# Kernel optimization log

Measured on AMD Instinct MI355X. Metric: run time of the kernel, lower is better.

Reference implementation:

```python
import jax, jax.numpy as jnp
import numpy as np

N_GENE = 50000
N_PROT = 50000
E = 500000
D = 128          # embedding_dim
C = 32           # out_channels = embedding_dim // attn_heads
F_IN = 256       # in_channels per node type
NUM_MP = 3       # metapaths: [gene-gene, gene-protein, protein-protein]


def _glorot(key, shape):
    lim = float(np.sqrt(6.0 / (shape[0] + shape[1])))
    return jax.random.uniform(key, shape, minval=-lim, maxval=lim, dtype=jnp.float32)


def setup_inputs() -> dict:
    key = jax.random.key(0)
    ks = jax.random.split(key, 24)
    inp = {
        "x_gene": jax.random.normal(ks[0], (N_GENE, F_IN), dtype=jnp.float32),
        "x_protein": jax.random.normal(ks[1], (N_PROT, F_IN), dtype=jnp.float32),
        # node-type projections linear_l / linear_r
        "Wl_gene": _glorot(ks[2], (D, F_IN)), "bl_gene": jnp.zeros((D,), jnp.float32),
        "Wr_gene": _glorot(ks[3], (D, F_IN)), "br_gene": jnp.zeros((D,), jnp.float32),
        "Wl_prot": _glorot(ks[4], (D, F_IN)), "bl_prot": jnp.zeros((D,), jnp.float32),
        "Wr_prot": _glorot(ks[5], (D, F_IN)), "br_prot": jnp.zeros((D,), jnp.float32),
        # per-metapath attention params (stacked over 3 metapaths)
        "alW": jnp.stack([_glorot(ks[6 + i], (C, D)) for i in range(NUM_MP)]),
        "alb": jnp.zeros((NUM_MP, C), jnp.float32),
        "arW": jnp.stack([_glorot(ks[9 + i], (C, D)) for i in range(NUM_MP)]),
        "arb": jnp.zeros((NUM_MP, C), jnp.float32),
        "qw": jnp.stack([_glorot(ks[12 + i], (2 * C, 1)) for i in range(NUM_MP)]),
        "sharp": jnp.ones((NUM_MP,), jnp.float32),  # 'sharpening' alpha_activation
        # per-node-type relation-weighting conv (Linear(D, 1))
        "conv_gene_W": _glorot(ks[15], (1, D)), "conv_gene_b": jnp.zeros((1,), jnp.float32),
        "conv_prot_W": _glorot(ks[16], (1, D)), "conv_prot_b": jnp.zeros((1,), jnp.float32),
        # edge indices: row 0 = head node (aggregation target), row 1 = tail node
        "edge_gg": jax.random.randint(ks[17], (2, E), 0, N_GENE, dtype=jnp.int32),
        "edge_gp": jnp.stack([jax.random.randint(ks[18], (E,), 0, N_GENE, dtype=jnp.int32),
                               jax.random.randint(ks[19], (E,), 0, N_PROT, dtype=jnp.int32)]),
        "edge_pp": jax.random.randint(ks[20], (2, E), 0, N_PROT, dtype=jnp.int32),
    }
    return inp


def _segment_softmax(scores, seg, n):
    # numerically stable softmax over variable-size neighborhoods (grouped by seg)
    m = jax.ops.segment_max(scores, seg, num_segments=n)
    m = jnp.where(jnp.isfinite(m), m, 0.0)
    ex = jnp.exp(scores - m[seg])
    denom = jax.ops.segment_sum(ex, seg, num_segments=n)
    return ex / (denom[seg] + 1e-16)


def _metapath_agg(l_head, r_tail, alW, alb, arW, arb, qw, sharp, eidx, n_head):
    # alpha_l / alpha_r node-level projections [N, C]
    al = l_head @ alW.T + alb
    ar = r_tail @ arW.T + arb
    src, dst = eidx[0], eidx[1]           # head (aggregate-at), tail (message-from)
    a_i = al[src]                          # [E, C]
    a_j = ar[dst]                          # [E, C]
    # attn_q: Tanh then Linear(2C -> 1, no bias); 'sharpening' scales the logit
    e = (jnp.tanh(jnp.concatenate([a_i, a_j], axis=1)) @ qw)[:, 0] * sharp  # [E]
    alpha = _segment_softmax(e, src, n_head)
    # message x_j * alpha, scatter-add into head nodes (aggr='add')
    return jax.ops.segment_sum(r_tail[dst] * alpha[:, None], src, num_segments=n_head)


def _relation_combine(aggs, l_self, conv_W, conv_b):
    # stack relation embeddings + self embedding: [N, R, D]
    out = jnp.stack(aggs + [l_self], axis=1)
    beta = jax.nn.softmax(out @ conv_W.T + conv_b, axis=1)  # [N, R, 1]
    return jax.nn.relu(jnp.sum(out * beta, axis=1))          # [N, D]


def reference(x_gene, x_protein, Wl_gene, bl_gene, Wr_gene, br_gene,
              Wl_prot, bl_prot, Wr_prot, br_prot,
              alW, alb, arW, arb, qw, sharp,
              conv_gene_W, conv_gene_b, conv_prot_W, conv_prot_b,
              edge_gg, edge_gp, edge_pp):
    # first layer: l/r projections from raw features
    l_gene = x_gene @ Wl_gene.T + bl_gene
    r_gene = x_gene @ Wr_gene.T + br_gene
    l_prot = x_protein @ Wl_prot.T + bl_prot
    r_prot = x_protein @ Wr_prot.T + br_prot

    # metapath 0: gene <- gene ; metapath 1: gene <- protein ; metapath 2: protein <- protein
    agg_gg = _metapath_agg(l_gene, r_gene, alW[0], alb[0], arW[0], arb[0], qw[0], sharp[0], edge_gg, N_GENE)
    agg_gp = _metapath_agg(l_gene, r_prot, alW[1], alb[1], arW[1], arb[1], qw[1], sharp[1], edge_gp, N_GENE)
    agg_pp = _metapath_agg(l_prot, r_prot, alW[2], alb[2], arW[2], arb[2], qw[2], sharp[2], edge_pp, N_PROT)

    out_gene = _relation_combine([agg_gg, agg_gp], l_gene, conv_gene_W, conv_gene_b)
    out_prot = _relation_combine([agg_pp], l_prot, conv_prot_W, conv_prot_b)
    return (out_gene, out_prot)
```

## Files before the change

### kernel.cpp

```cpp
#include <hip/hip_runtime.h>
#include <hip/hip_bf16.h>


typedef __attribute__((ext_vector_type(8))) short short8;
typedef __attribute__((ext_vector_type(4))) float floatx4;

__device__ __forceinline__ void gload16(const void* g, void* l) {
  __builtin_amdgcn_global_load_lds(
      (const __attribute__((address_space(1))) void*)g,
      (__attribute__((address_space(3))) void*)l, 16, 0, 0);
}

__device__ __forceinline__ ushort f2b(float x) {
  __hip_bfloat16 h = __float2bfloat16(x);
  return *reinterpret_cast<ushort*>(&h);
}
__device__ __forceinline__ float b2f_lo(unsigned v) { return __uint_as_float(v << 16); }
__device__ __forceinline__ float b2f_hi(unsigned v) { return __uint_as_float(v & 0xffff0000u); }

struct CvtArgs {
  const float* src[8];
  ushort* dst[8];
  int valid[8];
  int total[8];
  int bstart[9];
};
__global__ __launch_bounds__(256) void cvt_multi(CvtArgs a) {
  int b = blockIdx.x;
  int e = 0;
#pragma unroll
  for (int j = 1; j < 8; ++j)
    if (b >= a.bstart[j]) e = j;
  int i = ((b - a.bstart[e]) * 256 + threadIdx.x) * 4;
  if (i >= a.total[e]) return;
  float4 v = make_float4(0.f, 0.f, 0.f, 0.f);
  if (i < a.valid[e]) v = *(const float4*)(a.src[e] + i);
  ushort4 o;
  o.x = f2b(v.x); o.y = f2b(v.y); o.z = f2b(v.z); o.w = f2b(v.w);
  *(ushort4*)(a.dst[e] + i) = o;
}

struct ProjArgs {
  const float* x[2];
  const ushort* Wb[2];
  const float* bl[2];
  const float* br[2];
  ushort* lb[2];
  ushort* rb[2];
  int N[2];
};
__global__ __launch_bounds__(512) void proj_lr_mfma(ProjArgs g) {
  const int ty = blockIdx.y;
  const float* xp = g.x[ty];
  const int N = g.N[ty];
  __shared__ ushort As[128 * 32];
  __shared__ ushort Bs[256 * 32];
  const int tid = threadIdx.x;
  const int lane = tid & 63;
  const int wave = tid >> 6;
  const int wm = wave & 1, wn = wave >> 1;
  const int rowBase = blockIdx.x * 128;
  const ushort* Wb = g.Wb[ty];

  floatx4 acc[4][4] = {};

  const int arow = tid >> 2, achk = tid & 3;
  const int xrow = min(rowBase + arow, N - 1);
  const float* xrp = xp + (size_t)xrow * 256;

  for (int k0 = 0; k0 < 256; k0 += 32) {
#pragma unroll
    for (int i = 0; i < 2; ++i) {
      int t = tid + i * 512;
      gload16(Wb + (size_t)(t >> 2) * 256 + k0 + (t & 3) * 8, &Bs[t * 8]);
    }
    float4 lo = *(const float4*)(xrp + k0 + achk * 8);
    float4 hi = *(const float4*)(xrp + k0 + achk * 8 + 4);
    ushort4 c0, c1;
    c0.x = f2b(lo.x); c0.y = f2b(lo.y); c0.z = f2b(lo.z); c0.w = f2b(lo.w);
    c1.x = f2b(hi.x); c1.y = f2b(hi.y); c1.z = f2b(hi.z); c1.w = f2b(hi.w);
    *(ushort4*)&As[arow * 32 + achk * 8] = c0;
    *(ushort4*)&As[arow * 32 + achk * 8 + 4] = c1;
    __syncthreads();
    short8 bf[4];
#pragma unroll
    for (int nt = 0; nt < 4; ++nt)
      bf[nt] = *(const short8*)&Bs[(wn * 64 + nt * 16 + (lane & 15)) * 32 + (lane >> 4) * 8];
#pragma unroll
    for (int mt = 0; mt < 4; ++mt) {
      short8 a = *(const short8*)&As[(wm * 64 + mt * 16 + (lane & 15)) * 32 + (lane >> 4) * 8];
#pragma unroll
      for (int nt = 0; nt < 4; ++nt)
        acc[mt][nt] = __builtin_amdgcn_mfma_f32_16x16x32_bf16(a, bf[nt], acc[mt][nt], 0, 0, 0);
    }
    __syncthreads();
  }

#pragma unroll
  for (int mt = 0; mt < 4; ++mt)
#pragma unroll
    for (int nt = 0; nt < 4; ++nt) {
      const int col = wn * 64 + nt * 16 + (lane & 15);
      const int half = col >> 7, c = col & 127;
      const float bv = (half ? g.br[ty] : g.bl[ty])[c];
      ushort* outp = half ? g.rb[ty] : g.lb[ty];
#pragma unroll
      for (int vi = 0; vi < 4; ++vi) {
        int row = rowBase + wm * 64 + mt * 16 + (lane >> 4) * 4 + vi;
        if (row < N) outp[(size_t)row * 128 + c] = f2b(acc[mt][nt][vi] + bv);
      }
    }
}

struct AttnArgs {
  const ushort* Ab[4];
  const ushort* Wb[4];
  const float* bias[4];
  const float* q0[4];
  const float* q1[4];
  float* o0[4];
  float* o1[4];
  int N[4];
  int BN[4];
};
__global__ __launch_bounds__(256) void attn_proj_multi(AttnArgs g) {
  const int ei = blockIdx.y;
  const ushort* Ab = g.Ab[ei];
  const ushort* Wb = g.Wb[ei];
  const int N = g.N[ei], BN = g.BN[ei];
  const int NB = BN >> 4;
  __shared__ ushort As[128 * 32];
  __shared__ ushort Ws[64 * 128];
  const int tid = threadIdx.x;
  const int lane = tid & 63;
  const int wave = tid >> 6;
  const int rowBase = blockIdx.x * 128;

  for (int i = 0; i < NB; ++i) {
    int idx = tid + i * 256;
    gload16(Wb + (size_t)idx * 8, &Ws[idx * 8]);
  }

  floatx4 acc[2][4] = {};
  for (int k0 = 0; k0 < 128; k0 += 32) {
#pragma unroll
    for (int i = 0; i < 2; ++i) {
      int t = tid + i * 256;
      gload16(Ab + (size_t)(rowBase + (t >> 2)) * 128 + k0 + (t & 3) * 8, &As[t * 8]);
    }
    __syncthreads();
    short8 bf[4];
#pragma unroll
    for (int nt = 0; nt < 4; ++nt)
      if (nt < NB)
        bf[nt] = *(const short8*)&Ws[(nt * 16 + (lane & 15)) * 128 + k0 + (lane >> 4) * 8];
#pragma unroll
    for (int mt = 0; mt < 2; ++mt) {
      short8 a = *(const short8*)&As[(wave * 32 + mt * 16 + (lane & 15)) * 32 + (lane >> 4) * 8];
#pragma unroll
      for (int nt = 0; nt < 4; ++nt)
        if (nt < NB)
          acc[mt][nt] = __builtin_amdgcn_mfma_f32_16x16x32_bf16(a, bf[nt], acc[mt][nt], 0, 0, 0);
    }
    __syncthreads();
  }

  const float* bias = g.bias[ei];
  const int l15 = lane & 15;
  const bool two = (NB == 4);
  float bv[4];
#pragma unroll
  for (int nt = 0; nt < 4; ++nt) bv[nt] = (nt < NB) ? bias[nt * 16 + l15] : 0.f;
  float q0v0 = g.q0[ei][l15], q0v1 = g.q0[ei][16 + l15];
  float q1v0 = 0.f, q1v1 = 0.f;
  if (two) { q1v0 = g.q1[ei][l15]; q1v1 = g.q1[ei][16 + l15]; }
  float* o0 = g.o0[ei];
  float* o1 = g.o1[ei];
#pragma unroll
  for (int mt = 0; mt < 2; ++mt)
#pragma unroll
    for (int vi = 0; vi < 4; ++vi) {
      float slo = tanhf(acc[mt][0][vi] + bv[0]) * q0v0
                + tanhf(acc[mt][1][vi] + bv[1]) * q0v1;
      float shi = 0.f;
      if (two)
        shi = tanhf(acc[mt][2][vi] + bv[2]) * q1v0
            + tanhf(acc[mt][3][vi] + bv[3]) * q1v1;
#pragma unroll
      for (int m = 8; m >= 1; m >>= 1) {
        slo += __shfl_xor(slo, m, 64);
        shi += __shfl_xor(shi, m, 64);
      }
      const int row = rowBase + wave * 32 + mt * 16 + (lane >> 4) * 4 + vi;
      if (l15 == 0 && row < N) {
        o0[row] = slo;
        if (two) o1[row] = shi;
      }
    }
}

__global__ __launch_bounds__(256) void hist3_kernel(
    const int* __restrict__ e0, const int* __restrict__ e1,
    const int* __restrict__ e2, int* __restrict__ deg,
    int* __restrict__ rank, int E, int NG) {
  int e = blockIdx.x * 256 + threadIdx.x;
  if (e >= 3 * E) return;
  int mp = (e >= 2 * E) ? 2 : ((e >= E) ? 1 : 0);
  int el = e - mp * E;
  const int* ep = (mp == 0) ? e0 : (mp == 1) ? e1 : e2;
  int segb = (mp == 2) ? 2 * NG : mp * NG;
  rank[e] = atomicAdd(&deg[segb + ep[el]], 1);
}

__global__ __launch_bounds__(256) void scanA_kernel(
    const int* __restrict__ deg, int* __restrict__ offsets,
    int* __restrict__ tile_tot, int n) {
  __shared__ int wtot[4];
  const int t = threadIdx.x;
  const int base = blockIdx.x * 2048 + t * 8;
  int v[8], pre[8], s = 0;
#pragma unroll
  for (int j = 0; j < 8; ++j) {
    v[j] = (base + j < n) ? deg[base + j] : 0;
    pre[j] = s;
    s += v[j];
  }
  const int lane = t & 63, wv = t >> 6;
  int x = s;
#pragma unroll
  for (int o = 1; o < 64; o <<= 1) {
    int u = __shfl_up(x, o, 64);
    if (lane >= o) x += u;
  }
  if (lane == 63) wtot[wv] = x;
  __syncthreads();
  int wpre = 0;
#pragma unroll
  for (int j = 0; j < 4; ++j) wpre += (j < wv) ? wtot[j] : 0;
  int excl = wpre + x - s;
#pragma unroll
  for (int j = 0; j < 8; ++j)
    if (base + j < n) offsets[base + j] = excl + pre[j];
  if (t == 255) tile_tot[blockIdx.x] = wpre + x;
}

__global__ __launch_bounds__(256) void scanB_kernel(
    const int* __restrict__ tile_tot, int* __restrict__ tile_pre,
    int* __restrict__ offsets, int T, int n) {
  __shared__ int wtot[4];
  const int t = threadIdx.x;
  int v = (t < T) ? tile_tot[t] : 0;
  const int lane = t & 63, wv = t >> 6;
  int x = v;
#pragma unroll
  for (int o = 1; o < 64; o <<= 1) {
    int u = __shfl_up(x, o, 64);
    if (lane >= o) x += u;
  }
  if (lane == 63) wtot[wv] = x;
  __syncthreads();
  int wpre = 0;
#pragma unroll
  for (int j = 0; j < 4; ++j) wpre += (j < wv) ? wtot[j] : 0;
  if (t < T) tile_pre[t] = wpre + x - v;
  if (t == 255) offsets[n] = wpre + x;
}

__global__ __launch_bounds__(256) void scanC_kernel(
    int* __restrict__ offsets, const int* __restrict__ tile_pre, int n) {
  const int add = tile_pre[blockIdx.x];
  const int base = blockIdx.x * 2048 + threadIdx.x * 8;
#pragma unroll
  for (int j = 0; j < 8; ++j)
    if (base + j < n) offsets[base + j] += add;
}

__global__ __launch_bounds__(256) void scatter3_kernel(
    const int* __restrict__ e0, const int* __restrict__ e1,
    const int* __restrict__ e2, const int* __restrict__ rank,
    const int* __restrict__ offsets,
    const float* __restrict__ tl3, const float* __restrict__ tr3,
    const float* __restrict__ sharp, int2* __restrict__ recs,
    int E, int NG, int NP) {
  int e = blockIdx.x * 256 + threadIdx.x;
  if (e >= 3 * E) return;
  int mp = (e >= 2 * E) ? 2 : ((e >= E) ? 1 : 0);
  int el = e - mp * E;
  const int* ep = (mp == 0) ? e0 : (mp == 1) ? e1 : e2;
  int s = ep[el], d = ep[el + E];
  int hb = (mp == 2) ? 2 * NG : mp * NG;
  int tb = (mp == 0) ? 0 : (mp == 1) ? NG : NG + NP;
  float w = expf((tl3[hb + s] + tr3[tb + d]) * sharp[mp]);
  recs[offsets[hb + s] + rank[e]] = make_int2(d << 8, __float_as_int(w));
}

__global__ __launch_bounds__(256) void gather_combine(
    const ushort* __restrict__ rb_gene, const ushort* __restrict__ rb_prot,
    const ushort* __restrict__ lb_gene, const ushort* __restrict__ lb_prot,
    const int* __restrict__ offsets, const int2* __restrict__ recs,
    const float* __restrict__ cgW, const float* __restrict__ cgb,
    const float* __restrict__ cpW, const float* __restrict__ cpb,
    float* __restrict__ out_gene, float* __restrict__ out_prot,
    int NG, int NP) {
  const int lane = threadIdx.x & 63;
  const int l16 = lane & 15;
  const int node = blockIdx.x * 16 + (threadIdx.x >> 4);
  if (node >= NG + NP) return;
  const bool isGene = node < NG;
  const unsigned coloff = (unsigned)l16 << 4;
  const unsigned OMASK = 0x00FFFF00u;

  const int h0 = isGene ? node : NG + node;
  const int j0a = offsets[h0];
  const int ca = offsets[h0 + 1] - j0a;
  int j0b = 0, cb2 = 0;
  if (isGene) {
    j0b = offsets[NG + node];
    cb2 = offsets[NG + node + 1] - j0b;
  }

  float a0[8] = {0.f, 0.f, 0.f, 0.f, 0.f, 0.f, 0.f, 0.f};
  float a1[8] = {0.f, 0.f, 0.f, 0.f, 0.f, 0.f, 0.f, 0.f};
  float ds0 = 0.f, ds1 = 0.f;
  const ushort* rtA = isGene ? rb_gene : rb_prot;

  if (isGene) {
    const int cmax = (ca > cb2) ? ca : cb2;
    if (cmax > 0) {
      int2 rA[4], rB[4];
#pragma unroll
      for (int p = 0; p < 4; ++p) {
        rA[p] = recs[j0a + ((p < ca) ? p : 0)];
        rB[p] = recs[j0b + ((p < cb2) ? p : 0)];
      }
      const int nit = (cmax + 3) >> 2;
      for (int it = 0; it < nit; ++it) {
        const int b = it * 4;
        float wA[4], wB[4];
        uint4 vA[4], vB[4];
#pragma unroll
        for (int p = 0; p < 4; ++p) {
          wA[p] = (b + p < ca)  ? __int_as_float(rA[p].y) : 0.f;
          wB[p] = (b + p < cb2) ? __int_as_float(rB[p].y) : 0.f;
          vA[p] = *(const uint4*)((const char*)rtA + (((unsigned)rA[p].x & OMASK) + coloff));
          vB[p] = *(const uint4*)((const char*)rb_prot + (((unsigned)rB[p].x & OMASK) + coloff));
        }
        const int nb = b + 4;
#pragma unroll
        for (int p = 0; p < 4; ++p) {
          rA[p] = recs[j0a + ((nb + p < ca) ? nb + p : 0)];
          rB[p] = recs[j0b + ((nb + p < cb2) ? nb + p : 0)];
        }
#pragma unroll
        for (int p = 0; p < 4; ++p) {
          ds0 += wA[p];
          a0[0] += b2f_lo(vA[p].x) * wA[p]; a0[1] += b2f_hi(vA[p].x) * wA[p];
          a0[2] += b2f_lo(vA[p].y) * wA[p]; a0[3] += b2f_hi(vA[p].y) * wA[p];
          a0[4] += b2f_lo(vA[p].z) * wA[p]; a0[5] += b2f_hi(vA[p].z) * wA[p];
          a0[6] += b2f_lo(vA[p].w) * wA[p]; a0[7] += b2f_hi(vA[p].w) * wA[p];
          ds1 += wB[p];
          a1[0] += b2f_lo(vB[p].x) * wB[p]; a1[1] += b2f_hi(vB[p].x) * wB[p];
          a1[2] += b2f_lo(vB[p].y) * wB[p]; a1[3] += b2f_hi(vB[p].y) * wB[p];
          a1[4] += b2f_lo(vB[p].z) * wB[p]; a1[5] += b2f_hi(vB[p].z) * wB[p];
          a1[6] += b2f_lo(vB[p].w) * wB[p]; a1[7] += b2f_hi(vB[p].w) * wB[p];
        }
      }
    }
  } else {
    if (ca > 0) {
      int2 r0 = recs[j0a];
      int2 r1 = recs[j0a + ((1 < ca) ? 1 : 0)];
      int2 r2 = recs[j0a + ((2 < ca) ? 2 : 0)];
      int2 r3 = recs[j0a + ((3 < ca) ? 3 : 0)];
      const int nit = (ca + 3) >> 2;
      for (int it = 0; it < nit; ++it) {
        const int b = it * 4;
        const float w0 = (b < ca)     ? __int_as_float(r0.y) : 0.f;
        const float w1 = (b + 1 < ca) ? __int_as_float(r1.y) : 0.f;
        const float w2 = (b + 2 < ca) ? __int_as_float(r2.y) : 0.f;
        const float w3 = (b + 3 < ca) ? __int_as_float(r3.y) : 0.f;
        const uint4 v0 = *(const uint4*)((const char*)rtA + (((unsigned)r0.x & OMASK) + coloff));
        const uint4 v1 = *(const uint4*)((const char*)rtA + (((unsigned)r1.x & OMASK) + coloff));
        const uint4 v2 = *(const uint4*)((const char*)rtA + (((unsigned)r2.x & OMASK) + coloff));
        const uint4 v3 = *(const uint4*)((const char*)rtA + (((unsigned)r3.x & OMASK) + coloff));
        const int nb = b + 4;
        r0 = recs[j0a + ((nb < ca) ? nb : 0)];
        r1 = recs[j0a + ((nb + 1 < ca) ? nb + 1 : 0)];
        r2 = recs[j0a + ((nb + 2 < ca) ? nb + 2 : 0)];
        r3 = recs[j0a + ((nb + 3 < ca) ? nb + 3 : 0)];
        ds0 += (w0 + w1) + (w2 + w3);
        a0[0] += b2f_lo(v0.x) * w0 + b2f_lo(v1.x) * w1 + b2f_lo(v2.x) * w2 + b2f_lo(v3.x) * w3;
        a0[1] += b2f_hi(v0.x) * w0 + b2f_hi(v1.x) * w1 + b2f_hi(v2.x) * w2 + b2f_hi(v3.x) * w3;
        a0[2] += b2f_lo(v0.y) * w0 + b2f_lo(v1.y) * w1 + b2f_lo(v2.y) * w2 + b2f_lo(v3.y) * w3;
        a0[3] += b2f_hi(v0.y) * w0 + b2f_hi(v1.y) * w1 + b2f_hi(v2.y) * w2 + b2f_hi(v3.y) * w3;
        a0[4] += b2f_lo(v0.z) * w0 + b2f_lo(v1.z) * w1 + b2f_lo(v2.z) * w2 + b2f_lo(v3.z) * w3;
        a0[5] += b2f_hi(v0.z) * w0 + b2f_hi(v1.z) * w1 + b2f_hi(v2.z) * w2 + b2f_hi(v3.z) * w3;
        a0[6] += b2f_lo(v0.w) * w0 + b2f_lo(v1.w) * w1 + b2f_lo(v2.w) * w2 + b2f_lo(v3.w) * w3;
        a0[7] += b2f_hi(v0.w) * w0 + b2f_hi(v1.w) * w1 + b2f_hi(v2.w) * w2 + b2f_hi(v3.w) * w3;
      }
    }
  }

  const float inv0 = 1.f / (ds0 + 1e-16f);
  const float inv1 = 1.f / (ds1 + 1e-16f);
  float g0[8], g1[8], self[8];
#pragma unroll
  for (int c = 0; c < 8; ++c) { g0[c] = a0[c] * inv0; g1[c] = a1[c] * inv1; }
  {
    const ushort* lbp = isGene ? lb_gene + (size_t)node * 128
                               : lb_prot + (size_t)(node - NG) * 128;
    uint4 sv = *(const uint4*)(lbp + l16 * 8);
    self[0] = b2f_lo(sv.x); self[1] = b2f_hi(sv.x);
    self[2] = b2f_lo(sv.y); self[3] = b2f_hi(sv.y);
    self[4] = b2f_lo(sv.z); self[5] = b2f_hi(sv.z);
    self[6] = b2f_lo(sv.w); self[7] = b2f_hi(sv.w);
  }

  const float* cW = isGene ? cgW : cpW;
  const float cb = isGene ? cgb[0] : cpb[0];
  const float4 wlo = *(const float4*)(cW + l16 * 8);
  const float4 whi = *(const float4*)(cW + l16 * 8 + 4);
  float p0 = g0[0] * wlo.x + g0[1] * wlo.y + g0[2] * wlo.z + g0[3] * wlo.w +
             g0[4] * whi.x + g0[5] * whi.y + g0[6] * whi.z + g0[7] * whi.w;
  float p1 = g1[0] * wlo.x + g1[1] * wlo.y + g1[2] * wlo.z + g1[3] * wlo.w +
             g1[4] * whi.x + g1[5] * whi.y + g1[6] * whi.z + g1[7] * whi.w;
  float ps = self[0] * wlo.x + self[1] * wlo.y + self[2] * wlo.z + self[3] * wlo.w +
             self[4] * whi.x + self[5] * whi.y + self[6] * whi.z + self[7] * whi.w;
#pragma unroll
  for (int m = 8; m >= 1; m >>= 1) {
    p0 += __shfl_xor(p0, m, 64);
    p1 += __shfl_xor(p1, m, 64);
    ps += __shfl_xor(ps, m, 64);
  }
  const float s0 = p0 + cb, s1 = p1 + cb, ss = ps + cb;
  const float mx = isGene ? fmaxf(fmaxf(s0, s1), ss) : fmaxf(s0, ss);
  const float e0 = expf(s0 - mx);
  const float e1 = isGene ? expf(s1 - mx) : 0.f;
  const float es = expf(ss - mx);
  const float sum = e0 + e1 + es;
  const float b0 = e0 / sum, b1 = e1 / sum, bs = es / sum;

  float4 o0, o1;
  o0.x = fmaxf(g0[0] * b0 + g1[0] * b1 + self[0] * bs, 0.f);
  o0.y = fmaxf(g0[1] * b0 + g1[1] * b1 + self[1] * bs, 0.f);
  o0.z = fmaxf(g0[2] * b0 + g1[2] * b1 + self[2] * bs, 0.f);
  o0.w = fmaxf(g0[3] * b0 + g1[3] * b1 + self[3] * bs, 0.f);
  o1.x = fmaxf(g0[4] * b0 + g1[4] * b1 + self[4] * bs, 0.f);
  o1.y = fmaxf(g0[5] * b0 + g1[5] * b1 + self[5] * bs, 0.f);
  o1.z = fmaxf(g0[6] * b0 + g1[6] * b1 + self[6] * bs, 0.f);
  o1.w = fmaxf(g0[7] * b0 + g1[7] * b1 + self[7] * bs, 0.f);
  float* op = isGene ? out_gene + (size_t)node * 128
                     : out_prot + (size_t)(node - NG) * 128;
  *(float4*)(op + l16 * 8) = o0;
  *(float4*)(op + l16 * 8 + 4) = o1;
}

extern "C" void kernel_launch(void* const* d_in, const int* in_sizes, int n_in,
                              void* d_out, int out_size, void* d_ws,
                              size_t ws_size, hipStream_t stream) {
  const float* x_gene  = (const float*)d_in[0];
  const float* x_prot  = (const float*)d_in[1];
  const float* Wl_gene = (const float*)d_in[2];
  const float* bl_gene = (const float*)d_in[3];
  const float* Wr_gene = (const float*)d_in[4];
  const float* br_gene = (const float*)d_in[5];
  const float* Wl_prot = (const float*)d_in[6];
  const float* bl_prot = (const float*)d_in[7];
  const float* Wr_prot = (const float*)d_in[8];
  const float* br_prot = (const float*)d_in[9];
  const float* alW     = (const float*)d_in[10];
  const float* alb     = (const float*)d_in[11];
  const float* arW     = (const float*)d_in[12];
  const float* arb     = (const float*)d_in[13];
  const float* qw      = (const float*)d_in[14];
  const float* sharp   = (const float*)d_in[15];
  const float* cgW     = (const float*)d_in[16];
  const float* cgb     = (const float*)d_in[17];
  const float* cpW     = (const float*)d_in[18];
  const float* cpb     = (const float*)d_in[19];
  const int* e_gg      = (const int*)d_in[20];
  const int* e_gp      = (const int*)d_in[21];
  const int* e_pp      = (const int*)d_in[22];

  const int NG = in_sizes[0] / 256;
  const int NP = in_sizes[1] / 256;
  const int E  = in_sizes[20] / 2;
  const int NPG = (NG + 127) & ~127;
  const int NT = 2 * NG + NP;
  const int NR = NG + 2 * NP;

  char* base = (char*)d_ws;
  size_t off = 0;
  auto alloc = [&](size_t bytes) {
    void* p = base + off;
    off = (off + bytes + 255) & ~(size_t)255;
    return p;
  };
  ushort* Wlr_gene = (ushort*)alloc(256 * 256 * 2);
  ushort* Wlr_prot = (ushort*)alloc(256 * 256 * 2);
  ushort* alWb     = (ushort*)alloc(96 * 128 * 2);
  ushort* arWb     = (ushort*)alloc(96 * 128 * 2);
  ushort* lb_gene  = (ushort*)alloc((size_t)NPG * 128 * 2);
  ushort* rb_gene  = (ushort*)alloc((size_t)NPG * 128 * 2);
  ushort* lb_prot  = (ushort*)alloc((size_t)NPG * 128 * 2);
  ushort* rb_prot  = (ushort*)alloc((size_t)NPG * 128 * 2);
  int*    deg      = (int*)alloc((size_t)NT * 4);
  int*    offsets  = (int*)alloc((size_t)(NT + 1) * 4);
  const int TILES  = (NT + 2047) / 2048;
  int*    tile_tot = (int*)alloc((size_t)TILES * 4);
  int*    tile_pre = (int*)alloc((size_t)TILES * 4);
  int*    rank     = (int*)alloc((size_t)(3 * E) * 4);
  int2*   recs     = (int2*)alloc((size_t)(3 * E) * sizeof(int2));
  float*  tl3      = (float*)alloc((size_t)NT * 4);
  float*  tr3      = (float*)alloc((size_t)NR * 4);

  float* out_gene = (float*)d_out;
  float* out_prot = out_gene + (size_t)NG * 128;

  dim3 blk(256);

  {
    CvtArgs a;
    const float* srcs[8] = {Wl_gene, Wr_gene, Wl_prot, Wr_prot, alW, arW,
                            Wl_gene, Wl_gene};
    ushort* dsts[8] = {Wlr_gene, Wlr_gene + 128 * 256,
                       Wlr_prot, Wlr_prot + 128 * 256, alWb, arWb,
                       Wlr_gene, Wlr_gene};
    int sizes[8] = {128 * 256, 128 * 256, 128 * 256, 128 * 256,
                    96 * 128, 96 * 128, 0, 0};
    int b = 0;
    for (int j = 0; j < 8; ++j) {
      a.src[j] = srcs[j]; a.dst[j] = dsts[j];
      a.valid[j] = sizes[j]; a.total[j] = sizes[j];
      a.bstart[j] = b;
      b += (sizes[j] / 4 + 255) / 256;
    }
    a.bstart[8] = b;
    cvt_multi<<<b, blk, 0, stream>>>(a);
  }

  {
    ProjArgs p;
    p.x[0] = x_gene; p.x[1] = x_prot;
    p.Wb[0] = Wlr_gene; p.Wb[1] = Wlr_prot;
    p.bl[0] = bl_gene; p.bl[1] = bl_prot;
    p.br[0] = br_gene; p.br[1] = br_prot;
    p.lb[0] = lb_gene; p.lb[1] = lb_prot;
    p.rb[0] = rb_gene; p.rb[1] = rb_prot;
    p.N[0] = NG; p.N[1] = NP;
    proj_lr_mfma<<<dim3(NPG / 128, 2), dim3(512), 0, stream>>>(p);
  }

  {
    AttnArgs a;
    a.Ab[0] = lb_gene; a.Wb[0] = alWb;            a.bias[0] = alb;      a.N[0] = NG; a.BN[0] = 64;
    a.q0[0] = qw + 0;  a.q1[0] = qw + 64;  a.o0[0] = tl3;          a.o1[0] = tl3 + NG;
    a.Ab[1] = rb_gene; a.Wb[1] = arWb;            a.bias[1] = arb;      a.N[1] = NG; a.BN[1] = 32;
    a.q0[1] = qw + 32; a.q1[1] = qw + 32;  a.o0[1] = tr3;          a.o1[1] = tr3;
    a.Ab[2] = lb_prot; a.Wb[2] = alWb + 64 * 128; a.bias[2] = alb + 64; a.N[2] = NP; a.BN[2] = 32;
    a.q0[2] = qw + 128; a.q1[2] = qw + 128; a.o0[2] = tl3 + 2 * NG; a.o1[2] = tl3 + 2 * NG;
    a.Ab[3] = rb_prot; a.Wb[3] = arWb + 32 * 128; a.bias[3] = arb + 32; a.N[3] = NP; a.BN[3] = 64;
    a.q0[3] = qw + 96; a.q1[3] = qw + 160; a.o0[3] = tr3 + NG;     a.o1[3] = tr3 + NG + NP;
    attn_proj_multi<<<dim3(NPG / 128, 4), blk, 0, stream>>>(a);
  }

  const int gridE3 = (3 * E + 255) / 256;
  hipMemsetAsync(deg, 0, (size_t)NT * sizeof(int), stream);
  hist3_kernel<<<gridE3, blk, 0, stream>>>(e_gg, e_gp, e_pp, deg, rank, E, NG);
  scanA_kernel<<<TILES, blk, 0, stream>>>(deg, offsets, tile_tot, NT);
  scanB_kernel<<<1, blk, 0, stream>>>(tile_tot, tile_pre, offsets, TILES, NT);
  scanC_kernel<<<TILES, blk, 0, stream>>>(offsets, tile_pre, NT);
  scatter3_kernel<<<gridE3, blk, 0, stream>>>(e_gg, e_gp, e_pp, rank, offsets,
                                              tl3, tr3, sharp, recs, E, NG, NP);

  gather_combine<<<(NG + NP + 15) / 16, blk, 0, stream>>>(
      rb_gene, rb_prot, lb_gene, lb_prot, offsets, recs,
      cgW, cgb, cpW, cpb, out_gene, out_prot, NG, NP);
}
```

Baseline: 407.9 us.

## Split l/r projection GEMM into column halves and prefetch x rows

The projection kernel now launches separate blocks for the l and r output halves (256 threads, 128-column tile) instead of one 512-thread block computing all 256 columns. Each thread also loads its x-feature slice for the next k-step into registers before the barrier, so global load latency can overlap the MFMA work. The split gives twice as many smaller blocks for occupancy, but each fp32 x row is now read and converted to bf16 twice.

```diff
diff --git a/kernel.cpp b/kernel.cpp
--- a/kernel.cpp
+++ b/kernel.cpp
@@ -49,38 +49,55 @@
   ushort* rb[2];
   int N[2];
 };
-__global__ __launch_bounds__(512) void proj_lr_mfma(ProjArgs g) {
-  const int ty = blockIdx.y;
+__global__ __launch_bounds__(256) void proj_lr_mfma(ProjArgs g) {
+  const int ty = blockIdx.z;
   const float* xp = g.x[ty];
   const int N = g.N[ty];
   __shared__ ushort As[128 * 32];
-  __shared__ ushort Bs[256 * 32];
+  __shared__ ushort Bs[128 * 32];
   const int tid = threadIdx.x;
   const int lane = tid & 63;
   const int wave = tid >> 6;
   const int wm = wave & 1, wn = wave >> 1;
   const int rowBase = blockIdx.x * 128;
-  const ushort* Wb = g.Wb[ty];
+  const int colHalf = blockIdx.y;
+  const ushort* Wbase = g.Wb[ty] + (size_t)colHalf * 128 * 256;
 
   floatx4 acc[4][4] = {};
 
-  const int arow = tid >> 2, achk = tid & 3;
+  const int arow = tid >> 1, ahalf = tid & 1;
   const int xrow = min(rowBase + arow, N - 1);
-  const float* xrp = xp + (size_t)xrow * 256;
+  const float* xrp = xp + (size_t)xrow * 256 + ahalf * 16;
+
+  float4 px0 = *(const float4*)(xrp + 0);
+  float4 px1 = *(const float4*)(xrp + 4);
+  float4 px2 = *(const float4*)(xrp + 8);
+  float4 px3 = *(const float4*)(xrp + 12);
 
   for (int k0 = 0; k0 < 256; k0 += 32) {
 #pragma unroll
     for (int i = 0; i < 2; ++i) {
-      int t = tid + i * 512;
-      gload16(Wb + (size_t)(t >> 2) * 256 + k0 + (t & 3) * 8, &Bs[t * 8]);
-    }
-    float4 lo = *(const float4*)(xrp + k0 + achk * 8);
-    float4 hi = *(const float4*)(xrp + k0 + achk * 8 + 4);
-    ushort4 c0, c1;
-    c0.x = f2b(lo.x); c0.y = f2b(lo.y); c0.z = f2b(lo.z); c0.w = f2b(lo.w);
-    c1.x = f2b(hi.x); c1.y = f2b(hi.y); c1.z = f2b(hi.z); c1.w = f2b(hi.w);
-    *(ushort4*)&As[arow * 32 + achk * 8] = c0;
-    *(ushort4*)&As[arow * 32 + achk * 8 + 4] = c1;
+      int t = tid + i * 256;
+      gload16(Wbase + (size_t)(t >> 2) * 256 + k0 + (t & 3) * 8, &Bs[t * 8]);
+    }
+    ushort4 c0, c1, c2, c3;
+    c0.x = f2b(px0.x); c0.y = f2b(px0.y); c0.z = f2b(px0.z); c0.w = f2b(px0.w);
+    c1.x = f2b(px1.x); c1.y = f2b(px1.y); c1.z = f2b(px1.z); c1.w = f2b(px1.w);
+    c2.x = f2b(px2.x); c2.y = f2b(px2.y); c2.z = f2b(px2.z); c2.w = f2b(px2.w);
+    c3.x = f2b(px3.x); c3.y = f2b(px3.y); c3.z = f2b(px3.z); c3.w = f2b(px3.w);
+    {
+      ushort* ap = &As[arow * 32 + ahalf * 16];
+      *(ushort4*)(ap + 0) = c0;
+      *(ushort4*)(ap + 4) = c1;
+      *(ushort4*)(ap + 8) = c2;
+      *(ushort4*)(ap + 12) = c3;
+    }
+    if (k0 < 224) {
+      px0 = *(const float4*)(xrp + k0 + 32);
+      px1 = *(const float4*)(xrp + k0 + 36);
+      px2 = *(const float4*)(xrp + k0 + 40);
+      px3 = *(const float4*)(xrp + k0 + 44);
+    }
     __syncthreads();
     short8 bf[4];
 #pragma unroll
@@ -96,18 +113,18 @@
     __syncthreads();
   }
 
+  const float* bias = colHalf ? g.br[ty] : g.bl[ty];
+  ushort* outp = colHalf ? g.rb[ty] : g.lb[ty];
 #pragma unroll
   for (int mt = 0; mt < 4; ++mt)
 #pragma unroll
     for (int nt = 0; nt < 4; ++nt) {
-      const int col = wn * 64 + nt * 16 + (lane & 15);
-      const int half = col >> 7, c = col & 127;
-      const float bv = (half ? g.br[ty] : g.bl[ty])[c];
-      ushort* outp = half ? g.rb[ty] : g.lb[ty];
+      int col = wn * 64 + nt * 16 + (lane & 15);
+      float bv = bias[col];
 #pragma unroll
       for (int vi = 0; vi < 4; ++vi) {
         int row = rowBase + wm * 64 + mt * 16 + (lane >> 4) * 4 + vi;
-        if (row < N) outp[(size_t)row * 128 + c] = f2b(acc[mt][nt][vi] + bv);
+        if (row < N) outp[(size_t)row * 128 + col] = f2b(acc[mt][nt][vi] + bv);
       }
     }
 }
@@ -548,7 +565,7 @@
     p.lb[0] = lb_gene; p.lb[1] = lb_prot;
     p.rb[0] = rb_gene; p.rb[1] = rb_prot;
     p.N[0] = NG; p.N[1] = NP;
-    proj_lr_mfma<<<dim3(NPG / 128, 2), dim3(512), 0, stream>>>(p);
+    proj_lr_mfma<<<dim3(NPG / 128, 2, 2), blk, 0, stream>>>(p);
   }
 
   {
```

Result: no change. 414.3 us (+1.6%).
